# Kernel tuning notes

Hardware: AMD Instinct MI355X
Metric: run time of the kernel (lower is better)

Reference implementation:

```python
import jax, jax.numpy as jnp
import numpy as np

B, IN_SIZE, OUT_SIZE, N_QUBITS, DEPTH = 4096, 512, 256, 12, 3
C64 = jnp.complex64
BN_EPS = 1e-5


def setup_inputs() -> dict:
    key = jax.random.key(0)
    ks = jax.random.split(key, 6)
    x = jax.random.normal(ks[0], (B, IN_SIZE), jnp.float32)
    enc_w = jax.random.normal(ks[1], (N_QUBITS, IN_SIZE), jnp.float32) / np.sqrt(IN_SIZE)
    enc_b = jnp.zeros((N_QUBITS,), jnp.float32)
    rot_params = jax.random.normal(ks[2], (DEPTH, N_QUBITS, 3), jnp.float32) * 0.1
    ent_params = jax.random.normal(ks[3], (DEPTH, N_QUBITS - 1), jnp.float32) * 0.1
    dec_w = jax.random.normal(ks[4], (OUT_SIZE, N_QUBITS), jnp.float32) / np.sqrt(N_QUBITS)
    dec_b = jnp.zeros((OUT_SIZE,), jnp.float32)
    return {
        'x': x, 'enc_w': enc_w, 'enc_b': enc_b,
        'rot_params': rot_params, 'ent_params': ent_params,
        'dec_w': dec_w, 'dec_b': dec_b,
        'bn1_gamma': jnp.ones((N_QUBITS,), jnp.float32),
        'bn1_beta': jnp.zeros((N_QUBITS,), jnp.float32),
        'bn2_gamma': jnp.ones((OUT_SIZE,), jnp.float32),
        'bn2_beta': jnp.zeros((OUT_SIZE,), jnp.float32),
    }


def _m2(a, b, c, d):
    return jnp.stack([jnp.stack([a, b]), jnp.stack([c, d])]).astype(C64)


def _rx(t):
    c = jnp.cos(t / 2).astype(C64)
    s = jnp.sin(t / 2).astype(C64)
    return _m2(c, -1j * s, -1j * s, c)


def _ry(t):
    c = jnp.cos(t / 2)
    s = jnp.sin(t / 2)
    return _m2(c, -s, s, c)


def _rz(p):
    z = jnp.zeros((), C64)
    return _m2(jnp.exp(-1j * p / 2), z, z, jnp.exp(1j * p / 2))


def _apply_1q(state, U, q):
    # state: [B, 2^n]; apply 2x2 U on qubit q (qubit 0 = most significant axis)
    b = state.shape[0]
    s = state.reshape(b, 2 ** q, 2, -1)
    s = jnp.einsum('ij,bkjl->bkil', U, s)
    return s.reshape(b, -1)


def _apply_cry(state, theta, q):
    # controlled-Ry: control qubit q, target qubit q+1 (adjacent)
    b = state.shape[0]
    R = _ry(theta)
    st = state.reshape(b, 2 ** q, 2, 2, -1)
    s0 = st[:, :, 0]
    s1 = jnp.einsum('ij,bkjl->bkil', R, st[:, :, 1])
    return jnp.stack([s0, s1], axis=2).reshape(b, -1)


def _batchnorm(x, g, b):
    # BatchNorm1d in training mode: biased batch stats
    m = x.mean(0)
    v = x.var(0)
    return g * (x - m) / jnp.sqrt(v + BN_EPS) + b


def _quantum_forward(encoded, rot_params, ent_params):
    # Batched statevector simulation of the per-sample circuit.
    b, n = encoded.shape
    depth = rot_params.shape[0]
    # amplitude encoding: normalize, theta = 2*arcsin(clip(|a|,0,1)), P(pi) if a<0
    norm = jnp.linalg.norm(encoded, axis=1, keepdims=True)
    a = jnp.where(norm > 0, encoded / jnp.maximum(norm, 1e-30), encoded)
    amp = jnp.clip(jnp.abs(a), 0.0, 1.0)              # sin(theta/2)
    cos_h = jnp.sqrt(jnp.maximum(1.0 - amp * amp, 0.0))  # cos(theta/2)
    sgn = jnp.where(a < 0, -1.0, 1.0)                  # P(pi) flips sign of |1> amp
    qvec = jnp.stack([cos_h, sgn * amp], axis=-1).astype(C64)  # [B, n, 2]
    # product state via successive outer products (loop over fixed n qubits)
    state = jnp.ones((b, 1), C64)
    for q in range(n):
        state = (state[:, :, None] * qvec[:, q, None, :]).reshape(b, -1)
    # parameterized circuit
    for l in range(depth):
        for q in range(n):
            U = _rz(rot_params[l, q, 2]) @ _ry(rot_params[l, q, 1]) @ _rx(rot_params[l, q, 0])
            state = _apply_1q(state, U, q)
        for q in range(n - 1):
            state = _apply_cry(state, ent_params[l, q], q)
    # per-qubit P(|1>) measurement probabilities
    idx = jnp.arange(2 ** n)
    bits = ((idx[:, None] >> (n - 1 - jnp.arange(n))) & 1).astype(jnp.float32)  # [2^n, n]
    probs = (jnp.abs(state) ** 2).astype(jnp.float32) @ bits  # [B, n]
    return probs


def reference(x, enc_w, enc_b, rot_params, ent_params, dec_w, dec_b,
              bn1_gamma, bn1_beta, bn2_gamma, bn2_beta):
    encoded = x @ enc_w.T + enc_b
    encoded = jnp.tanh(_batchnorm(encoded, bn1_gamma, bn1_beta))
    probs = _quantum_forward(encoded, rot_params, ent_params)
    out = probs @ dec_w.T + dec_b
    return _batchnorm(out, bn2_gamma, bn2_beta)
```

## Files before the change

### kernel.cpp

```cpp
#include <hip/hip_runtime.h>

#define BATCH   4096
#define IN_SZ   512
#define NQ      12
#define OUT_SZ  256
#define DEPTH   3
#define NST     4096
#define BN_EPS  1e-5f

#define OFF_ENC    0
#define OFF_BN1M   49152
#define OFF_BN1R   49168
#define OFF_GU     49184
#define OFF_GC     49472
#define OFF_GF     49568
#define OFF_PROBS  49792
#define OFF_PMEAN  98944
#define OFF_COV    98960
#define OFF_RSTD   99104

typedef float v2f __attribute__((ext_vector_type(2)));
typedef float v4f __attribute__((ext_vector_type(4)));
#define SW2(a) __builtin_shufflevector(a, a, 1, 0)

__global__ void k_encode(const float* __restrict__ x, const float* __restrict__ w,
                         const float* __restrict__ bvec,
                         const float* __restrict__ rot, const float* __restrict__ ent,
                         float* __restrict__ enc, float* __restrict__ gU, float* __restrict__ gC,
                         float* __restrict__ gF) {
    if (blockIdx.x == 1024) {
        int t = threadIdx.x;
        if (t < DEPTH * NQ) {
            float ax = rot[t * 3 + 0] * 0.5f;
            float ay = rot[t * 3 + 1] * 0.5f;
            float az = rot[t * 3 + 2] * 0.5f;
            float cx = cosf(ax), sx = sinf(ax);
            float cy = cosf(ay), sy = sinf(ay);
            float cz = cosf(az), sz = sinf(az);
            float m00r =  cy * cx, m00i =  sy * sx;
            float m01r = -sy * cx, m01i = -cy * sx;
            float m10r =  sy * cx, m10i = -cy * sx;
            float m11r =  cy * cx, m11i = -sy * sx;
            float* o = gU + t * 8;
            o[0] = cz * m00r + sz * m00i;  o[1] = cz * m00i - sz * m00r;
            o[2] = cz * m01r + sz * m01i;  o[3] = cz * m01i - sz * m01r;
            o[4] = cz * m10r - sz * m10i;  o[5] = cz * m10i + sz * m10r;
            o[6] = cz * m11r - sz * m11i;  o[7] = cz * m11i + sz * m11r;
        }
        if (t >= 64 && t - 64 < DEPTH * (NQ - 1)) {
            int i = t - 64;
            float th = ent[i] * 0.5f;
            gC[i * 2 + 0] = cosf(th);
            gC[i * 2 + 1] = sinf(th);
        }
        if (t >= 128 && t - 128 < DEPTH * 9) {
            int i = t - 128;
            int l = i / 9, k = i % 9;
            int c = k + k / 3;
            int tq = c + 1;
            const float* rr = rot + (l * NQ + tq) * 3;
            float ax = rr[0] * 0.5f, ay = rr[1] * 0.5f, az = rr[2] * 0.5f;
            float cx = cosf(ax), sx = sinf(ax);
            float cy = cosf(ay), sy = sinf(ay);
            float cz = cosf(az), sz = sinf(az);
            float m00r =  cy * cx, m00i =  sy * sx;
            float m01r = -sy * cx, m01i = -cy * sx;
            float m10r =  sy * cx, m10i = -cy * sx;
            float m11r =  cy * cx, m11i = -sy * sx;
            float u0 = cz * m00r + sz * m00i, u1 = cz * m00i - sz * m00r;
            float u2 = cz * m01r + sz * m01i, u3 = cz * m01i - sz * m01r;
            float u4 = cz * m10r - sz * m10i, u5 = cz * m10i + sz * m10r;
            float u6 = cz * m11r - sz * m11i, u7 = cz * m11i + sz * m11r;
            float th = ent[l * (NQ - 1) + c] * 0.5f;
            float c_ = cosf(th), s_ = sinf(th);
            float* o = gF + i * 8;
            o[0] = c_ * u0 - s_ * u4;  o[1] = c_ * u1 - s_ * u5;
            o[2] = c_ * u2 - s_ * u6;  o[3] = c_ * u3 - s_ * u7;
            o[4] = s_ * u0 + c_ * u4;  o[5] = s_ * u1 + c_ * u5;
            o[6] = s_ * u2 + c_ * u6;  o[7] = s_ * u3 + c_ * u7;
        }
        return;
    }
    int t = threadIdx.x;
    int wv = t >> 6, lane = t & 63;
    int row = blockIdx.x * 4 + wv;
    const float4* xr = (const float4*)(x + row * IN_SZ) + lane * 2;
    float4 xa = xr[0], xb = xr[1];
    float acc[NQ];
    #pragma unroll
    for (int q = 0; q < NQ; q++) {
        const float4* wr = (const float4*)(w + q * IN_SZ) + lane * 2;
        float4 wa = wr[0], wb = wr[1];
        float d = xa.x*wa.x + xa.y*wa.y + xa.z*wa.z + xa.w*wa.w
                + xb.x*wb.x + xb.y*wb.y + xb.z*wb.z + xb.w*wb.w;
        #pragma unroll
        for (int o = 32; o > 0; o >>= 1) d += __shfl_down(d, o, 64);
        acc[q] = d;
    }
    if (lane == 0) {
        float* er = enc + row * NQ;
        #pragma unroll
        for (int q = 0; q < NQ; q++) er[q] = acc[q] + bvec[q];
    }
}

__device__ float blockAllSum(float v, float* scr) {
    #pragma unroll
    for (int o = 32; o > 0; o >>= 1) v += __shfl_down(v, o, 64);
    int lane = threadIdx.x & 63, w = threadIdx.x >> 6;
    __syncthreads();
    if (lane == 0) scr[w] = v;
    __syncthreads();
    return scr[0] + scr[1] + scr[2] + scr[3];
}

__global__ void k_bnstats(const float* __restrict__ xm, float* __restrict__ mo,
                          float* __restrict__ ro) {
    __shared__ float scr[32];
    int j = blockIdx.x, t = threadIdx.x;
    float s = 0.f, s2 = 0.f;
    for (int b = t; b < BATCH; b += 1024) {
        float v = xm[b * NQ + j];
        s += v; s2 += v * v;
    }
    #pragma unroll
    for (int o = 32; o > 0; o >>= 1) { s += __shfl_down(s, o, 64); s2 += __shfl_down(s2, o, 64); }
    int lane = t & 63, w = t >> 6;
    if (lane == 0) { scr[w] = s; scr[16 + w] = s2; }
    __syncthreads();
    if (t == 0) {
        float S = 0.f, S2 = 0.f;
        #pragma unroll
        for (int i = 0; i < 16; i++) { S += scr[i]; S2 += scr[16 + i]; }
        float mean = S / (float)BATCH;
        float var  = S2 / (float)BATCH - mean * mean;
        mo[j] = mean;
        ro[j] = 1.f / sqrtf(var + BN_EPS);
    }
}

#define SLA2(j) ((T << 4) | ((((j) ^ ((T >> 1) & 7))) << 1))
#define SLB(m)  (((T & 0xF0) << 4) | ((m) << 4) | ((T & 15) ^ ((m) & 14)))
#define SLC(m)  (((m) << 8) | (T ^ ((((T >> 5) & 7)) << 1)))

#define LDA(j, Ra, Rb) { v4f t_ = *(const v4f*)(xch + SLA2(j));                 \
    Ra = __builtin_shufflevector(t_, t_, 0, 1);                                 \
    Rb = __builtin_shufflevector(t_, t_, 2, 3); }
#define STA(j, Ra, Rb) { v4f t_ = __builtin_shufflevector(Ra, Rb, 0, 1, 2, 3);  \
    *(v4f*)(xch + SLA2(j)) = t_; }

#define LOADA do { LDA(0,s0,s1) LDA(1,s2,s3) LDA(2,s4,s5) LDA(3,s6,s7)          \
    LDA(4,s8,s9) LDA(5,s10,s11) LDA(6,s12,s13) LDA(7,s14,s15) } while (0)
#define STORA do { STA(0,s0,s1) STA(1,s2,s3) STA(2,s4,s5) STA(3,s6,s7)          \
    STA(4,s8,s9) STA(5,s10,s11) STA(6,s12,s13) STA(7,s14,s15) } while (0)

#define LOADW(SL) do {                                                          \
    s0=xch[SL(0)];  s1=xch[SL(1)];  s2=xch[SL(2)];  s3=xch[SL(3)];              \
    s4=xch[SL(4)];  s5=xch[SL(5)];  s6=xch[SL(6)];  s7=xch[SL(7)];              \
    s8=xch[SL(8)];  s9=xch[SL(9)];  s10=xch[SL(10)]; s11=xch[SL(11)];           \
    s12=xch[SL(12)]; s13=xch[SL(13)]; s14=xch[SL(14)]; s15=xch[SL(15)]; } while (0)
#define STORW(SL) do {                                                          \
    xch[SL(0)]=s0;  xch[SL(1)]=s1;  xch[SL(2)]=s2;  xch[SL(3)]=s3;              \
    xch[SL(4)]=s4;  xch[SL(5)]=s5;  xch[SL(6)]=s6;  xch[SL(7)]=s7;              \
    xch[SL(8)]=s8;  xch[SL(9)]=s9;  xch[SL(10)]=s10; xch[SL(11)]=s11;           \
    xch[SL(12)]=s12; xch[SL(13)]=s13; xch[SL(14)]=s14; xch[SL(15)]=s15; } while (0)

#define U_LOADP(uptr) const float* u_ = (uptr);                                  \
    v2f c00r = {u_[0], u_[0]}, c00i = {-u_[1], u_[1]};                           \
    v2f c01r = {u_[2], u_[2]}, c01i = {-u_[3], u_[3]};                           \
    v2f c10r = {u_[4], u_[4]}, c10i = {-u_[5], u_[5]};                           \
    v2f c11r = {u_[6], u_[6]}, c11i = {-u_[7], u_[7]};

#define U_LOADF(uptr) const float* f_ = (uptr);                                  \
    v2f d00r = {f_[0], f_[0]}, d00i = {-f_[1], f_[1]};                           \
    v2f d01r = {f_[2], f_[2]}, d01i = {-f_[3], f_[3]};                           \
    v2f d10r = {f_[4], f_[4]}, d10i = {-f_[5], f_[5]};                           \
    v2f d11r = {f_[6], f_[6]}, d11i = {-f_[7], f_[7]};

#define U_PAIRP(A, B) { v2f a0 = A, a1 = B, a0s = SW2(a0), a1s = SW2(a1);        \
    A = a0*c00r + a0s*c00i + a1*c01r + a1s*c01i;                                 \
    B = a0*c10r + a0s*c10i + a1*c11r + a1s*c11i; }

#define U_PAIRF(A, B) { v2f a0 = A, a1 = B, a0s = SW2(a0), a1s = SW2(a1);        \
    A = a0*d00r + a0s*d00i + a1*d01r + a1s*d01i;                                 \
    B = a0*d10r + a0s*d10i + a1*d11r + a1s*d11i; }

#define APPLY_U_K3(uptr) do { U_LOADP(uptr)                                      \
    U_PAIRP(s0,s8) U_PAIRP(s1,s9) U_PAIRP(s2,s10) U_PAIRP(s3,s11)                \
    U_PAIRP(s4,s12) U_PAIRP(s5,s13) U_PAIRP(s6,s14) U_PAIRP(s7,s15) } while (0)

#define APPLY_UF_K2(uP, uF) do { U_LOADP(uP) U_LOADF(uF)                         \
    U_PAIRP(s0,s4) U_PAIRP(s1,s5) U_PAIRP(s2,s6) U_PAIRP(s3,s7)                  \
    U_PAIRF(s8,s12) U_PAIRF(s9,s13) U_PAIRF(s10,s14) U_PAIRF(s11,s15) } while (0)
#define APPLY_UF_K1(uP, uF) do { U_LOADP(uP) U_LOADF(uF)                         \
    U_PAIRP(s0,s2) U_PAIRP(s1,s3) U_PAIRF(s4,s6) U_PAIRF(s5,s7)                  \
    U_PAIRP(s8,s10) U_PAIRP(s9,s11) U_PAIRF(s12,s14) U_PAIRF(s13,s15) } while (0)
#define APPLY_UF_K0(uP, uF) do { U_LOADP(uP) U_LOADF(uF)                         \
    U_PAIRP(s0,s1) U_PAIRF(s2,s3) U_PAIRP(s4,s5) U_PAIRF(s6,s7)                  \
    U_PAIRP(s8,s9) U_PAIRF(s10,s11) U_PAIRP(s12,s13) U_PAIRF(s14,s15) } while (0)

#define RY_PAIRP(A, B) { v2f a0 = A, a1 = B;                                     \
    A = a0*cc2 - a1*ss2;  B = a0*ss2 + a1*cc2; }

#define RYALL_K3(cc, ss) do { v2f cc2 = {(cc),(cc)}, ss2 = {(ss),(ss)};          \
    RY_PAIRP(s0,s8) RY_PAIRP(s1,s9) RY_PAIRP(s2,s10) RY_PAIRP(s3,s11)            \
    RY_PAIRP(s4,s12) RY_PAIRP(s5,s13) RY_PAIRP(s6,s14) RY_PAIRP(s7,s15) } while (0)

#define INITJC(SR, j) { SR.x = f * (((j)&8)?qs0:qc0) * (((j)&4)?qs1:qc1)         \
    * (((j)&2)?qs2:qc2) * (((j)&1)?qs3:qc3); SR.y = 0.f; }
#define PRJ(S) ((S).x*(S).x + (S).y*(S).y)
#define WREDUCE(v) { v += __shfl_down(v,32,64); v += __shfl_down(v,16,64);       \
    v += __shfl_down(v,8,64); v += __shfl_down(v,4,64);                          \
    v += __shfl_down(v,2,64); v += __shfl_down(v,1,64); }

#define MKQ(i) float qc##i, qs##i; {                                             \
    float h_ = h##i;                                                             \
    float a_ = nz ? h_ * rinv : h_;                                              \
    float amp_ = fminf(fabsf(a_), 1.f);                                          \
    qc##i = sqrtf(fmaxf(1.f - amp_ * amp_, 0.f));                                \
    qs##i = (a_ < 0.f) ? -amp_ : amp_; }

__launch_bounds__(256)
__global__ void k_quantum(const float* __restrict__ enc,
                          const float* __restrict__ bn1m, const float* __restrict__ bn1r,
                          const float* __restrict__ g1, const float* __restrict__ b1,
                          const float* __restrict__ gU, const float* __restrict__ gC,
                          const float* __restrict__ gF,
                          float* __restrict__ probs) {
    __shared__ __align__(16) v2f xch[NST];

    int T = threadIdx.x, b = blockIdx.x;

    const float* er = enc + b * NQ;
    float h0  = tanhf(g1[0]  * (er[0]  - bn1m[0])  * bn1r[0]  + b1[0]);
    float h1  = tanhf(g1[1]  * (er[1]  - bn1m[1])  * bn1r[1]  + b1[1]);
    float h2  = tanhf(g1[2]  * (er[2]  - bn1m[2])  * bn1r[2]  + b1[2]);
    float h3  = tanhf(g1[3]  * (er[3]  - bn1m[3])  * bn1r[3]  + b1[3]);
    float h4  = tanhf(g1[4]  * (er[4]  - bn1m[4])  * bn1r[4]  + b1[4]);
    float h5  = tanhf(g1[5]  * (er[5]  - bn1m[5])  * bn1r[5]  + b1[5]);
    float h6  = tanhf(g1[6]  * (er[6]  - bn1m[6])  * bn1r[6]  + b1[6]);
    float h7  = tanhf(g1[7]  * (er[7]  - bn1m[7])  * bn1r[7]  + b1[7]);
    float h8  = tanhf(g1[8]  * (er[8]  - bn1m[8])  * bn1r[8]  + b1[8]);
    float h9  = tanhf(g1[9]  * (er[9]  - bn1m[9])  * bn1r[9]  + b1[9]);
    float h10 = tanhf(g1[10] * (er[10] - bn1m[10]) * bn1r[10] + b1[10]);
    float h11 = tanhf(g1[11] * (er[11] - bn1m[11]) * bn1r[11] + b1[11]);
    float n2 = h0*h0+h1*h1+h2*h2+h3*h3+h4*h4+h5*h5+h6*h6+h7*h7
             + h8*h8+h9*h9+h10*h10+h11*h11;
    float norm = sqrtf(n2);
    bool  nz   = norm > 0.f;
    float rinv = 1.f / fmaxf(norm, 1e-30f);
    MKQ(0) MKQ(1) MKQ(2) MKQ(3) MKQ(4) MKQ(5) MKQ(6) MKQ(7)
    MKQ(8) MKQ(9) MKQ(10) MKQ(11)

    v2f s0, s1, s2, s3, s4, s5, s6, s7, s8, s9, s10, s11, s12, s13, s14, s15;

    {
        float f = ((T>>7)&1 ? qs4 : qc4) * ((T>>6)&1 ? qs5 : qc5)
                * ((T>>5)&1 ? qs6 : qc6) * ((T>>4)&1 ? qs7 : qc7)
                * ((T>>3)&1 ? qs8 : qc8) * ((T>>2)&1 ? qs9 : qc9)
                * ((T>>1)&1 ? qs10 : qc10) * ((T>>0)&1 ? qs11 : qc11);
        INITJC(s0,0)  INITJC(s1,1)  INITJC(s2,2)  INITJC(s3,3)
        INITJC(s4,4)  INITJC(s5,5)  INITJC(s6,6)  INITJC(s7,7)
        INITJC(s8,8)  INITJC(s9,9)  INITJC(s10,10) INITJC(s11,11)
        INITJC(s12,12) INITJC(s13,13) INITJC(s14,14) INITJC(s15,15)
        APPLY_U_K3(gU + 0 * 8);
        APPLY_UF_K2(gU + 1 * 8, gF + 0 * 8);
        APPLY_UF_K1(gU + 2 * 8, gF + 1 * 8);
        APPLY_UF_K0(gU + 3 * 8, gF + 2 * 8);
        STORW(SLC);
    }
    __syncthreads();

    #pragma unroll 1
    for (int l = 0; l < DEPTH; l++) {
        const float* UL = gU + l * 96;
        const float* CL = gC + l * 22;
        const float* FL = gF + l * 72;
        LOADW(SLB);
        APPLY_U_K3(UL + 4 * 8);
        if (T & 16) RYALL_K3(CL[6], CL[7]);
        APPLY_UF_K2(UL + 5 * 8, FL + 3 * 8);
        APPLY_UF_K1(UL + 6 * 8, FL + 4 * 8);
        APPLY_UF_K0(UL + 7 * 8, FL + 5 * 8);
        STORW(SLB);
        __builtin_amdgcn_wave_barrier();
        LOADA;
        APPLY_U_K3(UL + 8 * 8);
        if (T & 1) RYALL_K3(CL[14], CL[15]);
        APPLY_UF_K2(UL + 9 * 8, FL + 6 * 8);
        APPLY_UF_K1(UL + 10 * 8, FL + 7 * 8);
        APPLY_UF_K0(UL + 11 * 8, FL + 8 * 8);
        if (l < DEPTH - 1) {
            STORA;
            __syncthreads();
            const float* UN = gU + (l + 1) * 96;
            const float* FN = gF + (l + 1) * 72;
            LOADW(SLC);
            APPLY_U_K3(UN + 0 * 8);
            APPLY_UF_K2(UN + 1 * 8, FN + 0 * 8);
            APPLY_UF_K1(UN + 2 * 8, FN + 1 * 8);
            APPLY_UF_K0(UN + 3 * 8, FN + 2 * 8);
            STORW(SLC);
            __syncthreads();
        }
    }

    float p0 = PRJ(s0),  p1 = PRJ(s1),  p2 = PRJ(s2),  p3 = PRJ(s3);
    float p4 = PRJ(s4),  p5 = PRJ(s5),  p6 = PRJ(s6),  p7 = PRJ(s7);
    float p8 = PRJ(s8),  p9 = PRJ(s9),  p10 = PRJ(s10), p11 = PRJ(s11);
    float p12 = PRJ(s12), p13 = PRJ(s13), p14 = PRJ(s14), p15 = PRJ(s15);
    float tot = p0+p1+p2+p3+p4+p5+p6+p7+p8+p9+p10+p11+p12+p13+p14+p15;
    float r8  = p8+p9+p10+p11+p12+p13+p14+p15;
    float r9  = p4+p5+p6+p7+p12+p13+p14+p15;
    float r10 = p2+p3+p6+p7+p10+p11+p14+p15;
    float r11 = p1+p3+p5+p7+p9+p11+p13+p15;
    float r0 = (T & 128) ? tot : 0.f;
    float r1 = (T & 64)  ? tot : 0.f;
    float r2 = (T & 32)  ? tot : 0.f;
    float r3 = (T & 16)  ? tot : 0.f;
    float r4 = (T & 8)   ? tot : 0.f;
    float r5 = (T & 4)   ? tot : 0.f;
    float r6 = (T & 2)   ? tot : 0.f;
    float r7 = (T & 1)   ? tot : 0.f;

    WREDUCE(r0) WREDUCE(r1) WREDUCE(r2) WREDUCE(r3) WREDUCE(r4) WREDUCE(r5)
    WREDUCE(r6) WREDUCE(r7) WREDUCE(r8) WREDUCE(r9) WREDUCE(r10) WREDUCE(r11)

    __syncthreads();
    float* red = (float*)xch;
    int lane = T & 63, w = T >> 6;
    if (lane == 0) {
        float* rr = red + w * NQ;
        rr[0]=r0; rr[1]=r1; rr[2]=r2; rr[3]=r3; rr[4]=r4; rr[5]=r5;
        rr[6]=r6; rr[7]=r7; rr[8]=r8; rr[9]=r9; rr[10]=r10; rr[11]=r11;
    }
    __syncthreads();
    if (T < NQ) probs[b * NQ + T] = red[T] + red[NQ + T] + red[2 * NQ + T] + red[3 * NQ + T];
}

__global__ void k_pcov(const float* __restrict__ probs, float* __restrict__ pmean,
                       float* __restrict__ cov) {
    __shared__ float scr[8];
    int blk = blockIdx.x;
    int q = blk / NQ, q2 = blk % NQ;
    int t = threadIdx.x;
    float sx = 0.f, sy = 0.f, sxy = 0.f;
    for (int b = t; b < BATCH; b += 256) {
        float xv = probs[b * NQ + q];
        float yv = probs[b * NQ + q2];
        sx += xv; sy += yv; sxy += xv * yv;
    }
    float SX  = blockAllSum(sx,  scr);
    float SY  = blockAllSum(sy,  scr);
    float SXY = blockAllSum(sxy, scr);
    if (t == 0) {
        float mx = SX / (float)BATCH, my = SY / (float)BATCH;
        cov[blk] = SXY / (float)BATCH - mx * my;
        if (q == q2) pmean[q] = mx;
    }
}

__global__ void k_rstd(const float* __restrict__ cov, const float* __restrict__ dw,
                       float* __restrict__ rstd) {
    __shared__ float cv[NQ * NQ];
    int t = threadIdx.x;
    if (t < NQ * NQ) cv[t] = cov[t];
    __syncthreads();
    float w[NQ];
    #pragma unroll
    for (int q = 0; q < NQ; q++) w[q] = dw[t * NQ + q];
    float var = 0.f;
    #pragma unroll
    for (int q = 0; q < NQ; q++) {
        float a = 0.f;
        #pragma unroll
        for (int q2 = 0; q2 < NQ; q2++) a += cv[q * NQ + q2] * w[q2];
        var += w[q] * a;
    }
    rstd[t] = 1.f / sqrtf(var + BN_EPS);
}

__global__ void k_final(const float* __restrict__ probs, const float* __restrict__ pmean,
                        const float* __restrict__ rstd, const float* __restrict__ dw,
                        const float* __restrict__ g2, const float* __restrict__ b2,
                        float* __restrict__ out) {
    __shared__ float cp[2][NQ];
    int b0 = blockIdx.x * 2;
    int t = threadIdx.x;
    int half = t >> 8, j = t & 255;
    if (t < NQ)                      cp[0][t]       = probs[b0 * NQ + t]        - pmean[t];
    else if (t >= 256 && t < 256+NQ) cp[1][t - 256] = probs[(b0+1) * NQ + t-256] - pmean[t - 256];
    __syncthreads();
    float acc = 0.f;
    #pragma unroll
    for (int q = 0; q < NQ; q++) acc += cp[half][q] * dw[j * NQ + q];
    out[(b0 + half) * OUT_SZ + j] = acc * rstd[j] * g2[j] + b2[j];
}

extern "C" void kernel_launch(void* const* d_in, const int* in_sizes, int n_in,
                              void* d_out, int out_size, void* d_ws, size_t ws_size,
                              hipStream_t stream) {
    const float* x     = (const float*)d_in[0];
    const float* enc_w = (const float*)d_in[1];
    const float* enc_b = (const float*)d_in[2];
    const float* rot   = (const float*)d_in[3];
    const float* ent   = (const float*)d_in[4];
    const float* dec_w = (const float*)d_in[5];
    const float* g1    = (const float*)d_in[7];
    const float* b1    = (const float*)d_in[8];
    const float* g2    = (const float*)d_in[9];
    const float* b2    = (const float*)d_in[10];

    float* ws    = (float*)d_ws;
    float* enc   = ws + OFF_ENC;
    float* bn1m  = ws + OFF_BN1M;
    float* bn1r  = ws + OFF_BN1R;
    float* gU    = ws + OFF_GU;
    float* gC    = ws + OFF_GC;
    float* gF    = ws + OFF_GF;
    float* prb   = ws + OFF_PROBS;
    float* pmean = ws + OFF_PMEAN;
    float* cov   = ws + OFF_COV;
    float* rstd  = ws + OFF_RSTD;

    hipLaunchKernelGGL(k_encode, dim3(1025), dim3(256), 0, stream,
                       x, enc_w, enc_b, rot, ent, enc, gU, gC, gF);
    hipLaunchKernelGGL(k_bnstats, dim3(NQ), dim3(1024), 0, stream, enc, bn1m, bn1r);
    hipLaunchKernelGGL(k_quantum, dim3(BATCH), dim3(256), 0, stream,
                       enc, bn1m, bn1r, g1, b1, gU, gC, gF, prb);
    hipLaunchKernelGGL(k_pcov, dim3(NQ * NQ), dim3(256), 0, stream, prb, pmean, cov);
    hipLaunchKernelGGL(k_rstd, dim3(1), dim3(OUT_SZ), 0, stream, cov, dec_w, rstd);
    hipLaunchKernelGGL(k_final, dim3(BATCH / 2), dim3(512), 0, stream,
                       prb, pmean, rstd, dec_w, g2, b2, (float*)d_out);
}
```

Baseline: 207.0 us.

## Fuse probability covariance into quantum kernel via atomics and pre-duplicate gate coefficients

Drops the separate k_pcov kernel. Each k_quantum block now atomically adds its 12 probabilities and 78 pairwise products into a 90-entry accumulator, which k_encode zeroes, and k_rstd rebuilds means and covariance from those sums. Gate matrices and CRY cos/sin are also stored pre-duplicated and sign-adjusted as v2f pairs, so the quantum kernel loads its coefficient vectors directly instead of building them. This saves one launch and the covariance pass over probs, at the cost of 4096×90 float atomics on a few addresses and results that depend on atomic ordering.

```diff
diff --git a/kernel.cpp b/kernel.cpp
--- a/kernel.cpp
+++ b/kernel.cpp
@@ -7,78 +7,81 @@
 #define DEPTH   3
 #define NST     4096
 #define BN_EPS  1e-5f
+#define INV_B   (1.f / 4096.f)
 
 #define OFF_ENC    0
 #define OFF_BN1M   49152
 #define OFF_BN1R   49168
-#define OFF_GU     49184
-#define OFF_GC     49472
-#define OFF_GF     49568
-#define OFF_PROBS  49792
-#define OFF_PMEAN  98944
-#define OFF_COV    98960
-#define OFF_RSTD   99104
+#define OFF_GU2    49184
+#define OFF_GC2    49760
+#define OFF_GF2    49920
+#define OFF_PROBS  50352
+#define OFF_ACC90  99504
+#define OFF_RSTD   99600
+#define OFF_PMEAN  99856
 
 typedef float v2f __attribute__((ext_vector_type(2)));
 typedef float v4f __attribute__((ext_vector_type(4)));
 #define SW2(a) __builtin_shufflevector(a, a, 1, 0)
 
+__device__ __forceinline__ void make_u(const float* rr, float* u) {
+    float ax = rr[0] * 0.5f, ay = rr[1] * 0.5f, az = rr[2] * 0.5f;
+    float cx = cosf(ax), sx = sinf(ax);
+    float cy = cosf(ay), sy = sinf(ay);
+    float cz = cosf(az), sz = sinf(az);
+    float m00r =  cy * cx, m00i =  sy * sx;
+    float m01r = -sy * cx, m01i = -cy * sx;
+    float m10r =  sy * cx, m10i = -cy * sx;
+    float m11r =  cy * cx, m11i = -sy * sx;
+    u[0] = cz * m00r + sz * m00i;  u[1] = cz * m00i - sz * m00r;
+    u[2] = cz * m01r + sz * m01i;  u[3] = cz * m01i - sz * m01r;
+    u[4] = cz * m10r - sz * m10i;  u[5] = cz * m10i + sz * m10r;
+    u[6] = cz * m11r - sz * m11i;  u[7] = cz * m11i + sz * m11r;
+}
+
+__device__ __forceinline__ void store_dup(float* o, const float* u) {
+    o[0] = u[0];  o[1] = u[0];   o[2] = -u[1];  o[3] = u[1];
+    o[4] = u[2];  o[5] = u[2];   o[6] = -u[3];  o[7] = u[3];
+    o[8] = u[4];  o[9] = u[4];   o[10] = -u[5]; o[11] = u[5];
+    o[12] = u[6]; o[13] = u[6];  o[14] = -u[7]; o[15] = u[7];
+}
+
 __global__ void k_encode(const float* __restrict__ x, const float* __restrict__ w,
                          const float* __restrict__ bvec,
                          const float* __restrict__ rot, const float* __restrict__ ent,
-                         float* __restrict__ enc, float* __restrict__ gU, float* __restrict__ gC,
-                         float* __restrict__ gF) {
+                         float* __restrict__ enc, float* __restrict__ gU2,
+                         float* __restrict__ gC2, float* __restrict__ gF2,
+                         float* __restrict__ acc90) {
     if (blockIdx.x == 1024) {
         int t = threadIdx.x;
         if (t < DEPTH * NQ) {
-            float ax = rot[t * 3 + 0] * 0.5f;
-            float ay = rot[t * 3 + 1] * 0.5f;
-            float az = rot[t * 3 + 2] * 0.5f;
-            float cx = cosf(ax), sx = sinf(ax);
-            float cy = cosf(ay), sy = sinf(ay);
-            float cz = cosf(az), sz = sinf(az);
-            float m00r =  cy * cx, m00i =  sy * sx;
-            float m01r = -sy * cx, m01i = -cy * sx;
-            float m10r =  sy * cx, m10i = -cy * sx;
-            float m11r =  cy * cx, m11i = -sy * sx;
-            float* o = gU + t * 8;
-            o[0] = cz * m00r + sz * m00i;  o[1] = cz * m00i - sz * m00r;
-            o[2] = cz * m01r + sz * m01i;  o[3] = cz * m01i - sz * m01r;
-            o[4] = cz * m10r - sz * m10i;  o[5] = cz * m10i + sz * m10r;
-            o[6] = cz * m11r - sz * m11i;  o[7] = cz * m11i + sz * m11r;
+            float u[8];
+            make_u(rot + t * 3, u);
+            store_dup(gU2 + t * 16, u);
         }
         if (t >= 64 && t - 64 < DEPTH * (NQ - 1)) {
             int i = t - 64;
             float th = ent[i] * 0.5f;
-            gC[i * 2 + 0] = cosf(th);
-            gC[i * 2 + 1] = sinf(th);
+            float c = cosf(th), s = sinf(th);
+            float* o = gC2 + i * 4;
+            o[0] = c; o[1] = c; o[2] = s; o[3] = s;
         }
         if (t >= 128 && t - 128 < DEPTH * 9) {
             int i = t - 128;
             int l = i / 9, k = i % 9;
             int c = k + k / 3;
-            int tq = c + 1;
-            const float* rr = rot + (l * NQ + tq) * 3;
-            float ax = rr[0] * 0.5f, ay = rr[1] * 0.5f, az = rr[2] * 0.5f;
-            float cx = cosf(ax), sx = sinf(ax);
-            float cy = cosf(ay), sy = sinf(ay);
-            float cz = cosf(az), sz = sinf(az);
-            float m00r =  cy * cx, m00i =  sy * sx;
-            float m01r = -sy * cx, m01i = -cy * sx;
-            float m10r =  sy * cx, m10i = -cy * sx;
-            float m11r =  cy * cx, m11i = -sy * sx;
-            float u0 = cz * m00r + sz * m00i, u1 = cz * m00i - sz * m00r;
-            float u2 = cz * m01r + sz * m01i, u3 = cz * m01i - sz * m01r;
-            float u4 = cz * m10r - sz * m10i, u5 = cz * m10i + sz * m10r;
-            float u6 = cz * m11r - sz * m11i, u7 = cz * m11i + sz * m11r;
+            float u[8];
+            make_u(rot + (l * NQ + c + 1) * 3, u);
             float th = ent[l * (NQ - 1) + c] * 0.5f;
             float c_ = cosf(th), s_ = sinf(th);
-            float* o = gF + i * 8;
-            o[0] = c_ * u0 - s_ * u4;  o[1] = c_ * u1 - s_ * u5;
-            o[2] = c_ * u2 - s_ * u6;  o[3] = c_ * u3 - s_ * u7;
-            o[4] = s_ * u0 + c_ * u4;  o[5] = s_ * u1 + c_ * u5;
-            o[6] = s_ * u2 + c_ * u6;  o[7] = s_ * u3 + c_ * u7;
+            float f[8];
+            f[0] = c_ * u[0] - s_ * u[4];  f[1] = c_ * u[1] - s_ * u[5];
+            f[2] = c_ * u[2] - s_ * u[6];  f[3] = c_ * u[3] - s_ * u[7];
+            f[4] = s_ * u[0] + c_ * u[4];  f[5] = s_ * u[1] + c_ * u[5];
+            f[6] = s_ * u[2] + c_ * u[6];  f[7] = s_ * u[3] + c_ * u[7];
+            store_dup(gF2 + i * 16, f);
         }
+        if (t >= 160 && t - 160 < 90) acc90[t - 160] = 0.f;
         return;
     }
     int t = threadIdx.x;
@@ -165,22 +168,16 @@
     xch[SL(8)]=s8;  xch[SL(9)]=s9;  xch[SL(10)]=s10; xch[SL(11)]=s11;           \
     xch[SL(12)]=s12; xch[SL(13)]=s13; xch[SL(14)]=s14; xch[SL(15)]=s15; } while (0)
 
-#define U_LOADP(uptr) const float* u_ = (uptr);                                  \
-    v2f c00r = {u_[0], u_[0]}, c00i = {-u_[1], u_[1]};                           \
-    v2f c01r = {u_[2], u_[2]}, c01i = {-u_[3], u_[3]};                           \
-    v2f c10r = {u_[4], u_[4]}, c10i = {-u_[5], u_[5]};                           \
-    v2f c11r = {u_[6], u_[6]}, c11i = {-u_[7], u_[7]};
-
-#define U_LOADF(uptr) const float* f_ = (uptr);                                  \
-    v2f d00r = {f_[0], f_[0]}, d00i = {-f_[1], f_[1]};                           \
-    v2f d01r = {f_[2], f_[2]}, d01i = {-f_[3], f_[3]};                           \
-    v2f d10r = {f_[4], f_[4]}, d10i = {-f_[5], f_[5]};                           \
-    v2f d11r = {f_[6], f_[6]}, d11i = {-f_[7], f_[7]};
+#define U_LOADP(uptr) const v2f* u_ = (const v2f*)(uptr);                        \
+    v2f c00r = u_[0], c00i = u_[1], c01r = u_[2], c01i = u_[3],                  \
+        c10r = u_[4], c10i = u_[5], c11r = u_[6], c11i = u_[7];
+#define U_LOADF(uptr) const v2f* f_ = (const v2f*)(uptr);                        \
+    v2f d00r = f_[0], d00i = f_[1], d01r = f_[2], d01i = f_[3],                  \
+        d10r = f_[4], d10i = f_[5], d11r = f_[6], d11i = f_[7];
 
 #define U_PAIRP(A, B) { v2f a0 = A, a1 = B, a0s = SW2(a0), a1s = SW2(a1);        \
     A = a0*c00r + a0s*c00i + a1*c01r + a1s*c01i;                                 \
     B = a0*c10r + a0s*c10i + a1*c11r + a1s*c11i; }
-
 #define U_PAIRF(A, B) { v2f a0 = A, a1 = B, a0s = SW2(a0), a1s = SW2(a1);        \
     A = a0*d00r + a0s*d00i + a1*d01r + a1s*d01i;                                 \
     B = a0*d10r + a0s*d10i + a1*d11r + a1s*d11i; }
@@ -201,8 +198,8 @@
 
 #define RY_PAIRP(A, B) { v2f a0 = A, a1 = B;                                     \
     A = a0*cc2 - a1*ss2;  B = a0*ss2 + a1*cc2; }
-
-#define RYALL_K3(cc, ss) do { v2f cc2 = {(cc),(cc)}, ss2 = {(ss),(ss)};          \
+#define RYALL_K3(cptr) do { const v2f* cp_ = (const v2f*)(cptr);                 \
+    v2f cc2 = cp_[0], ss2 = cp_[1];                                              \
     RY_PAIRP(s0,s8) RY_PAIRP(s1,s9) RY_PAIRP(s2,s10) RY_PAIRP(s3,s11)            \
     RY_PAIRP(s4,s12) RY_PAIRP(s5,s13) RY_PAIRP(s6,s14) RY_PAIRP(s7,s15) } while (0)
 
@@ -224,9 +221,9 @@
 __global__ void k_quantum(const float* __restrict__ enc,
                           const float* __restrict__ bn1m, const float* __restrict__ bn1r,
                           const float* __restrict__ g1, const float* __restrict__ b1,
-                          const float* __restrict__ gU, const float* __restrict__ gC,
-                          const float* __restrict__ gF,
-                          float* __restrict__ probs) {
+                          const float* __restrict__ gU2, const float* __restrict__ gC2,
+                          const float* __restrict__ gF2,
+                          float* __restrict__ probs, float* __restrict__ acc90) {
     __shared__ __align__(16) v2f xch[NST];
 
     int T = threadIdx.x, b = blockIdx.x;
@@ -263,43 +260,43 @@
         INITJC(s4,4)  INITJC(s5,5)  INITJC(s6,6)  INITJC(s7,7)
         INITJC(s8,8)  INITJC(s9,9)  INITJC(s10,10) INITJC(s11,11)
         INITJC(s12,12) INITJC(s13,13) INITJC(s14,14) INITJC(s15,15)
-        APPLY_U_K3(gU + 0 * 8);
-        APPLY_UF_K2(gU + 1 * 8, gF + 0 * 8);
-        APPLY_UF_K1(gU + 2 * 8, gF + 1 * 8);
-        APPLY_UF_K0(gU + 3 * 8, gF + 2 * 8);
+        APPLY_U_K3(gU2 + 0 * 16);
+        APPLY_UF_K2(gU2 + 1 * 16, gF2 + 0 * 16);
+        APPLY_UF_K1(gU2 + 2 * 16, gF2 + 1 * 16);
+        APPLY_UF_K0(gU2 + 3 * 16, gF2 + 2 * 16);
         STORW(SLC);
     }
     __syncthreads();
 
     #pragma unroll 1
     for (int l = 0; l < DEPTH; l++) {
-        const float* UL = gU + l * 96;
-        const float* CL = gC + l * 22;
-        const float* FL = gF + l * 72;
+        const float* UL = gU2 + l * 192;
+        const float* CL = gC2 + l * 44;
+        const float* FL = gF2 + l * 144;
         LOADW(SLB);
-        APPLY_U_K3(UL + 4 * 8);
-        if (T & 16) RYALL_K3(CL[6], CL[7]);
-        APPLY_UF_K2(UL + 5 * 8, FL + 3 * 8);
-        APPLY_UF_K1(UL + 6 * 8, FL + 4 * 8);
-        APPLY_UF_K0(UL + 7 * 8, FL + 5 * 8);
+        APPLY_U_K3(UL + 4 * 16);
+        if (T & 16) RYALL_K3(CL + 3 * 4);
+        APPLY_UF_K2(UL + 5 * 16, FL + 3 * 16);
+        APPLY_UF_K1(UL + 6 * 16, FL + 4 * 16);
+        APPLY_UF_K0(UL + 7 * 16, FL + 5 * 16);
         STORW(SLB);
         __builtin_amdgcn_wave_barrier();
         LOADA;
-        APPLY_U_K3(UL + 8 * 8);
-        if (T & 1) RYALL_K3(CL[14], CL[15]);
-        APPLY_UF_K2(UL + 9 * 8, FL + 6 * 8);
-        APPLY_UF_K1(UL + 10 * 8, FL + 7 * 8);
-        APPLY_UF_K0(UL + 11 * 8, FL + 8 * 8);
+        APPLY_U_K3(UL + 8 * 16);
+        if (T & 1) RYALL_K3(CL + 7 * 4);
+        APPLY_UF_K2(UL + 9 * 16, FL + 6 * 16);
+        APPLY_UF_K1(UL + 10 * 16, FL + 7 * 16);
+        APPLY_UF_K0(UL + 11 * 16, FL + 8 * 16);
         if (l < DEPTH - 1) {
             STORA;
             __syncthreads();
-            const float* UN = gU + (l + 1) * 96;
-            const float* FN = gF + (l + 1) * 72;
+            const float* UN = gU2 + (l + 1) * 192;
+            const float* FN = gF2 + (l + 1) * 144;
             LOADW(SLC);
-            APPLY_U_K3(UN + 0 * 8);
-            APPLY_UF_K2(UN + 1 * 8, FN + 0 * 8);
-            APPLY_UF_K1(UN + 2 * 8, FN + 1 * 8);
-            APPLY_UF_K0(UN + 3 * 8, FN + 2 * 8);
+            APPLY_U_K3(UN + 0 * 16);
+            APPLY_UF_K2(UN + 1 * 16, FN + 0 * 16);
+            APPLY_UF_K1(UN + 2 * 16, FN + 1 * 16);
+            APPLY_UF_K0(UN + 3 * 16, FN + 2 * 16);
             STORW(SLC);
             __syncthreads();
         }
@@ -335,36 +332,43 @@
         rr[6]=r6; rr[7]=r7; rr[8]=r8; rr[9]=r9; rr[10]=r10; rr[11]=r11;
     }
     __syncthreads();
-    if (T < NQ) probs[b * NQ + T] = red[T] + red[NQ + T] + red[2 * NQ + T] + red[3 * NQ + T];
-}
-
-__global__ void k_pcov(const float* __restrict__ probs, float* __restrict__ pmean,
-                       float* __restrict__ cov) {
-    __shared__ float scr[8];
-    int blk = blockIdx.x;
-    int q = blk / NQ, q2 = blk % NQ;
-    int t = threadIdx.x;
-    float sx = 0.f, sy = 0.f, sxy = 0.f;
-    for (int b = t; b < BATCH; b += 256) {
-        float xv = probs[b * NQ + q];
-        float yv = probs[b * NQ + q2];
-        sx += xv; sy += yv; sxy += xv * yv;
-    }
-    float SX  = blockAllSum(sx,  scr);
-    float SY  = blockAllSum(sy,  scr);
-    float SXY = blockAllSum(sxy, scr);
-    if (t == 0) {
-        float mx = SX / (float)BATCH, my = SY / (float)BATCH;
-        cov[blk] = SXY / (float)BATCH - mx * my;
-        if (q == q2) pmean[q] = mx;
-    }
-}
-
-__global__ void k_rstd(const float* __restrict__ cov, const float* __restrict__ dw,
-                       float* __restrict__ rstd) {
+    float* pq = red + 64;
+    if (T < NQ) {
+        float v = red[T] + red[NQ + T] + red[2 * NQ + T] + red[3 * NQ + T];
+        probs[b * NQ + T] = v;
+        pq[T] = v;
+    }
+    __syncthreads();
+    if (T < 90) {
+        float v;
+        if (T < NQ) {
+            v = pq[T];
+        } else {
+            int j = T - NQ, q = 0;
+            while (j >= NQ - q) { j -= NQ - q; q++; }
+            v = pq[q] * pq[q + j];
+        }
+        unsafeAtomicAdd(acc90 + T, v);
+    }
+}
+
+__global__ void k_rstd(const float* __restrict__ acc90, const float* __restrict__ dw,
+                       float* __restrict__ pmean, float* __restrict__ rstd) {
+    __shared__ float pm[NQ];
     __shared__ float cv[NQ * NQ];
     int t = threadIdx.x;
-    if (t < NQ * NQ) cv[t] = cov[t];
+    if (t < NQ) {
+        float m = acc90[t] * INV_B;
+        pm[t] = m;
+        pmean[t] = m;
+    }
+    __syncthreads();
+    if (t < NQ * NQ) {
+        int q = t / NQ, q2 = t - q * NQ;
+        int lo = q < q2 ? q : q2, hi = q < q2 ? q2 : q;
+        float P = acc90[NQ + lo * NQ - (lo * (lo - 1)) / 2 + (hi - lo)];
+        cv[t] = P * INV_B - pm[q] * pm[q2];
+    }
     __syncthreads();
     float w[NQ];
     #pragma unroll
@@ -415,21 +419,21 @@
     float* enc   = ws + OFF_ENC;
     float* bn1m  = ws + OFF_BN1M;
     float* bn1r  = ws + OFF_BN1R;
-    float* gU    = ws + OFF_GU;
-    float* gC    = ws + OFF_GC;
-    float* gF    = ws + OFF_GF;
+    float* gU2   = ws + OFF_GU2;
+    float* gC2   = ws + OFF_GC2;
+    float* gF2   = ws + OFF_GF2;
     float* prb   = ws + OFF_PROBS;
+    float* acc90 = ws + OFF_ACC90;
+    float* rstd  = ws + OFF_RSTD;
     float* pmean = ws + OFF_PMEAN;
-    float* cov   = ws + OFF_COV;
-    float* rstd  = ws + OFF_RSTD;
 
     hipLaunchKernelGGL(k_encode, dim3(1025), dim3(256), 0, stream,
-                       x, enc_w, enc_b, rot, ent, enc, gU, gC, gF);
+                       x, enc_w, enc_b, rot, ent, enc, gU2, gC2, gF2, acc90);
     hipLaunchKernelGGL(k_bnstats, dim3(NQ), dim3(1024), 0, stream, enc, bn1m, bn1r);
     hipLaunchKernelGGL(k_quantum, dim3(BATCH), dim3(256), 0, stream,
-                       enc, bn1m, bn1r, g1, b1, gU, gC, gF, prb);
-    hipLaunchKernelGGL(k_pcov, dim3(NQ * NQ), dim3(256), 0, stream, prb, pmean, cov);
-    hipLaunchKernelGGL(k_rstd, dim3(1), dim3(OUT_SZ), 0, stream, cov, dec_w, rstd);
+                       enc, bn1m, bn1r, g1, b1, gU2, gC2, gF2, prb, acc90);
+    hipLaunchKernelGGL(k_rstd, dim3(1), dim3(OUT_SZ), 0, stream,
+                       acc90, dec_w, pmean, rstd);
     hipLaunchKernelGGL(k_final, dim3(BATCH / 2), dim3(512), 0, stream,
                        prb, pmean, rstd, dec_w, g2, b2, (float*)d_out);
 }
```

New measurement: 219.8 us. 1.06x slower.

## Fuse probability covariance accumulation into quantum kernel via atomics

Applied to the files above, without the earlier changes.

Removes the separate k_pcov kernel. Each k_quantum block now atomically adds its 12 probabilities and 78 pairwise products into a 90-entry global accumulator, which the encode kernel zeroes. k_rstd rebuilds the means and covariance from those sums. This saves a kernel launch and a second pass over probs, but adds 4096×90 float atomics to a few addresses, which may contend, and the float summation order is no longer deterministic.

```diff
diff --git a/kernel.cpp b/kernel.cpp
--- a/kernel.cpp
+++ b/kernel.cpp
@@ -7,6 +7,7 @@
 #define DEPTH   3
 #define NST     4096
 #define BN_EPS  1e-5f
+#define INV_B   (1.f / 4096.f)
 
 #define OFF_ENC    0
 #define OFF_BN1M   49152
@@ -15,37 +16,42 @@
 #define OFF_GC     49472
 #define OFF_GF     49568
 #define OFF_PROBS  49792
-#define OFF_PMEAN  98944
-#define OFF_COV    98960
-#define OFF_RSTD   99104
+#define OFF_ACC90  98944
+#define OFF_RSTD   99040
+#define OFF_PMEAN  99296
 
 typedef float v2f __attribute__((ext_vector_type(2)));
 typedef float v4f __attribute__((ext_vector_type(4)));
 #define SW2(a) __builtin_shufflevector(a, a, 1, 0)
+
+__device__ __forceinline__ void make_u(const float* rr, float* u) {
+    float ax = rr[0] * 0.5f, ay = rr[1] * 0.5f, az = rr[2] * 0.5f;
+    float cx = cosf(ax), sx = sinf(ax);
+    float cy = cosf(ay), sy = sinf(ay);
+    float cz = cosf(az), sz = sinf(az);
+    float m00r =  cy * cx, m00i =  sy * sx;
+    float m01r = -sy * cx, m01i = -cy * sx;
+    float m10r =  sy * cx, m10i = -cy * sx;
+    float m11r =  cy * cx, m11i = -sy * sx;
+    u[0] = cz * m00r + sz * m00i;  u[1] = cz * m00i - sz * m00r;
+    u[2] = cz * m01r + sz * m01i;  u[3] = cz * m01i - sz * m01r;
+    u[4] = cz * m10r - sz * m10i;  u[5] = cz * m10i + sz * m10r;
+    u[6] = cz * m11r - sz * m11i;  u[7] = cz * m11i + sz * m11r;
+}
 
 __global__ void k_encode(const float* __restrict__ x, const float* __restrict__ w,
                          const float* __restrict__ bvec,
                          const float* __restrict__ rot, const float* __restrict__ ent,
                          float* __restrict__ enc, float* __restrict__ gU, float* __restrict__ gC,
-                         float* __restrict__ gF) {
+                         float* __restrict__ gF, float* __restrict__ acc90) {
     if (blockIdx.x == 1024) {
         int t = threadIdx.x;
         if (t < DEPTH * NQ) {
-            float ax = rot[t * 3 + 0] * 0.5f;
-            float ay = rot[t * 3 + 1] * 0.5f;
-            float az = rot[t * 3 + 2] * 0.5f;
-            float cx = cosf(ax), sx = sinf(ax);
-            float cy = cosf(ay), sy = sinf(ay);
-            float cz = cosf(az), sz = sinf(az);
-            float m00r =  cy * cx, m00i =  sy * sx;
-            float m01r = -sy * cx, m01i = -cy * sx;
-            float m10r =  sy * cx, m10i = -cy * sx;
-            float m11r =  cy * cx, m11i = -sy * sx;
+            float u[8];
+            make_u(rot + t * 3, u);
             float* o = gU + t * 8;
-            o[0] = cz * m00r + sz * m00i;  o[1] = cz * m00i - sz * m00r;
-            o[2] = cz * m01r + sz * m01i;  o[3] = cz * m01i - sz * m01r;
-            o[4] = cz * m10r - sz * m10i;  o[5] = cz * m10i + sz * m10r;
-            o[6] = cz * m11r - sz * m11i;  o[7] = cz * m11i + sz * m11r;
+            #pragma unroll
+            for (int i = 0; i < 8; i++) o[i] = u[i];
         }
         if (t >= 64 && t - 64 < DEPTH * (NQ - 1)) {
             int i = t - 64;
@@ -57,28 +63,17 @@
             int i = t - 128;
             int l = i / 9, k = i % 9;
             int c = k + k / 3;
-            int tq = c + 1;
-            const float* rr = rot + (l * NQ + tq) * 3;
-            float ax = rr[0] * 0.5f, ay = rr[1] * 0.5f, az = rr[2] * 0.5f;
-            float cx = cosf(ax), sx = sinf(ax);
-            float cy = cosf(ay), sy = sinf(ay);
-            float cz = cosf(az), sz = sinf(az);
-            float m00r =  cy * cx, m00i =  sy * sx;
-            float m01r = -sy * cx, m01i = -cy * sx;
-            float m10r =  sy * cx, m10i = -cy * sx;
-            float m11r =  cy * cx, m11i = -sy * sx;
-            float u0 = cz * m00r + sz * m00i, u1 = cz * m00i - sz * m00r;
-            float u2 = cz * m01r + sz * m01i, u3 = cz * m01i - sz * m01r;
-            float u4 = cz * m10r - sz * m10i, u5 = cz * m10i + sz * m10r;
-            float u6 = cz * m11r - sz * m11i, u7 = cz * m11i + sz * m11r;
+            float u[8];
+            make_u(rot + (l * NQ + c + 1) * 3, u);
             float th = ent[l * (NQ - 1) + c] * 0.5f;
             float c_ = cosf(th), s_ = sinf(th);
             float* o = gF + i * 8;
-            o[0] = c_ * u0 - s_ * u4;  o[1] = c_ * u1 - s_ * u5;
-            o[2] = c_ * u2 - s_ * u6;  o[3] = c_ * u3 - s_ * u7;
-            o[4] = s_ * u0 + c_ * u4;  o[5] = s_ * u1 + c_ * u5;
-            o[6] = s_ * u2 + c_ * u6;  o[7] = s_ * u3 + c_ * u7;
+            o[0] = c_ * u[0] - s_ * u[4];  o[1] = c_ * u[1] - s_ * u[5];
+            o[2] = c_ * u[2] - s_ * u[6];  o[3] = c_ * u[3] - s_ * u[7];
+            o[4] = s_ * u[0] + c_ * u[4];  o[5] = s_ * u[1] + c_ * u[5];
+            o[6] = s_ * u[2] + c_ * u[6];  o[7] = s_ * u[3] + c_ * u[7];
         }
+        if (t >= 160 && t - 160 < 90) acc90[t - 160] = 0.f;
         return;
     }
     int t = threadIdx.x;
@@ -226,7 +221,7 @@
                           const float* __restrict__ g1, const float* __restrict__ b1,
                           const float* __restrict__ gU, const float* __restrict__ gC,
                           const float* __restrict__ gF,
-                          float* __restrict__ probs) {
+                          float* __restrict__ probs, float* __restrict__ acc90) {
     __shared__ __align__(16) v2f xch[NST];
 
     int T = threadIdx.x, b = blockIdx.x;
@@ -335,36 +330,43 @@
         rr[6]=r6; rr[7]=r7; rr[8]=r8; rr[9]=r9; rr[10]=r10; rr[11]=r11;
     }
     __syncthreads();
-    if (T < NQ) probs[b * NQ + T] = red[T] + red[NQ + T] + red[2 * NQ + T] + red[3 * NQ + T];
-}
-
-__global__ void k_pcov(const float* __restrict__ probs, float* __restrict__ pmean,
-                       float* __restrict__ cov) {
-    __shared__ float scr[8];
-    int blk = blockIdx.x;
-    int q = blk / NQ, q2 = blk % NQ;
-    int t = threadIdx.x;
-    float sx = 0.f, sy = 0.f, sxy = 0.f;
-    for (int b = t; b < BATCH; b += 256) {
-        float xv = probs[b * NQ + q];
-        float yv = probs[b * NQ + q2];
-        sx += xv; sy += yv; sxy += xv * yv;
-    }
-    float SX  = blockAllSum(sx,  scr);
-    float SY  = blockAllSum(sy,  scr);
-    float SXY = blockAllSum(sxy, scr);
-    if (t == 0) {
-        float mx = SX / (float)BATCH, my = SY / (float)BATCH;
-        cov[blk] = SXY / (float)BATCH - mx * my;
-        if (q == q2) pmean[q] = mx;
-    }
-}
-
-__global__ void k_rstd(const float* __restrict__ cov, const float* __restrict__ dw,
-                       float* __restrict__ rstd) {
+    float* pq = red + 64;
+    if (T < NQ) {
+        float v = red[T] + red[NQ + T] + red[2 * NQ + T] + red[3 * NQ + T];
+        probs[b * NQ + T] = v;
+        pq[T] = v;
+    }
+    __syncthreads();
+    if (T < 90) {
+        float v;
+        if (T < NQ) {
+            v = pq[T];
+        } else {
+            int j = T - NQ, q = 0;
+            while (j >= NQ - q) { j -= NQ - q; q++; }
+            v = pq[q] * pq[q + j];
+        }
+        unsafeAtomicAdd(acc90 + T, v);
+    }
+}
+
+__global__ void k_rstd(const float* __restrict__ acc90, const float* __restrict__ dw,
+                       float* __restrict__ pmean, float* __restrict__ rstd) {
+    __shared__ float pm[NQ];
     __shared__ float cv[NQ * NQ];
     int t = threadIdx.x;
-    if (t < NQ * NQ) cv[t] = cov[t];
+    if (t < NQ) {
+        float m = acc90[t] * INV_B;
+        pm[t] = m;
+        pmean[t] = m;
+    }
+    __syncthreads();
+    if (t < NQ * NQ) {
+        int q = t / NQ, q2 = t - q * NQ;
+        int lo = q < q2 ? q : q2, hi = q < q2 ? q2 : q;
+        float P = acc90[NQ + lo * NQ - (lo * (lo - 1)) / 2 + (hi - lo)];
+        cv[t] = P * INV_B - pm[q] * pm[q2];
+    }
     __syncthreads();
     float w[NQ];
     #pragma unroll
@@ -419,17 +421,17 @@
     float* gC    = ws + OFF_GC;
     float* gF    = ws + OFF_GF;
     float* prb   = ws + OFF_PROBS;
+    float* acc90 = ws + OFF_ACC90;
+    float* rstd  = ws + OFF_RSTD;
     float* pmean = ws + OFF_PMEAN;
-    float* cov   = ws + OFF_COV;
-    float* rstd  = ws + OFF_RSTD;
 
     hipLaunchKernelGGL(k_encode, dim3(1025), dim3(256), 0, stream,
-                       x, enc_w, enc_b, rot, ent, enc, gU, gC, gF);
+                       x, enc_w, enc_b, rot, ent, enc, gU, gC, gF, acc90);
     hipLaunchKernelGGL(k_bnstats, dim3(NQ), dim3(1024), 0, stream, enc, bn1m, bn1r);
     hipLaunchKernelGGL(k_quantum, dim3(BATCH), dim3(256), 0, stream,
-                       enc, bn1m, bn1r, g1, b1, gU, gC, gF, prb);
-    hipLaunchKernelGGL(k_pcov, dim3(NQ * NQ), dim3(256), 0, stream, prb, pmean, cov);
-    hipLaunchKernelGGL(k_rstd, dim3(1), dim3(OUT_SZ), 0, stream, cov, dec_w, rstd);
+                       enc, bn1m, bn1r, g1, b1, gU, gC, gF, prb, acc90);
+    hipLaunchKernelGGL(k_rstd, dim3(1), dim3(OUT_SZ), 0, stream,
+                       acc90, dec_w, pmean, rstd);
     hipLaunchKernelGGL(k_final, dim3(BATCH / 2), dim3(512), 0, stream,
                        prb, pmean, rstd, dec_w, g2, b2, (float*)d_out);
 }
```

Result: slower. 215.6 us (+4.1%).
